# Performance work log

Hardware: AMD Instinct MI355X
Metric: run time of the kernel (lower is better)

The kernel has to match this reference:

```python
import jax, jax.numpy as jnp
import numpy as np

KERNEL = 7
PAD = 3
STRIDE = 1
DIL = 1
HEADS = 8
OUT_CH = 256


def _unfold(x, k, pad, stride, dil):
    # x: (B, C, H, W) -> (B, C*k*k, Ho, Wo); channel ordering (C, kh, kw),
    # matching torch.nn.Unfold's channel-major layout.
    return jax.lax.conv_general_dilated_patches(
        x, filter_shape=(k, k), window_strides=(stride, stride),
        padding=((pad, pad), (pad, pad)), rhs_dilation=(dil, dil))


def _conv1x1(x, w, b):
    # 1x1 conv == per-pixel matmul. w: (O, C), b: (O,)
    return jnp.einsum('bchw,oc->bohw', x, w) + b[None, :, None, None]


def setup_inputs() -> dict:
    key = jax.random.key(0)
    ks = jax.random.split(key, 11)
    B, C, H, W = 2, 256, 64, 64
    f = lambda k, sh: jax.random.normal(k, sh, dtype=jnp.float32)
    ws = 1.0 / np.sqrt(C).astype(np.float32)
    return dict(
        queries=f(ks[0], (B, C, H, W)),
        keys=f(ks[1], (B, C, H, W)),
        values=f(ks[2], (B, C, H, W)),
        wq=f(ks[3], (OUT_CH, C)) * ws, bq=f(ks[4], (OUT_CH,)) * 0.01,
        wk=f(ks[5], (OUT_CH, C)) * ws, bk=f(ks[6], (OUT_CH,)) * 0.01,
        wv=f(ks[7], (OUT_CH, C)) * ws, bv=f(ks[8], (OUT_CH,)) * 0.01,
        wo=f(ks[9], (OUT_CH, OUT_CH)) * ws, bo=f(ks[10], (OUT_CH,)) * 0.01,
    )


def reference(queries, keys, values, wq, bq, wk, bk, wv, bv, wo, bo):
    B = values.shape[0]
    d = OUT_CH // HEADS
    K2 = KERNEL * KERNEL
    q = _conv1x1(queries, wq, bq)
    k = _conv1x1(keys, wk, bk)
    v = _conv1x1(values, wv, bv)
    # query 'unfold' with kernel 1, stride STRIDE == strided subsample
    q = q[:, :, ::STRIDE, ::STRIDE]
    Ho, Wo = q.shape[-2], q.shape[-1]
    L = Ho * Wo
    q = q.reshape(B, HEADS, d, L)                                  # (B,h,d,L)
    kp = _unfold(k, KERNEL, PAD, STRIDE, DIL).reshape(B, HEADS, d, K2, L)
    vp = _unfold(v, KERNEL, PAD, STRIDE, DIL).reshape(B, HEADS, d, K2, L)
    scale = jnp.float32(1.0 / np.sqrt(OUT_CH))                     # note: sqrt(out_channels), per source
    attn = jnp.einsum('bhdl,bhdkl->bhlk', q, kp) * scale           # (B,h,L,K2)
    attn = jax.nn.softmax(attn, axis=-1)
    out = jnp.einsum('bhdkl,bhlk->bhdl', vp, attn)                 # (B,h,d,L)
    out = out.reshape(B, OUT_CH, Ho, Wo)
    return _conv1x1(out, wo, bo)
```

## Files before the change

### kernel.cpp

```cpp
#include <hip/hip_runtime.h>
#include <hip/hip_fp16.h>
#include <math.h>

#define B_ 2
#define C_ 256
#define H_ 64
#define W_ 64
#define L_ 4096
#define HEADS_ 8
#define DH_ 32
#define CG_ 8
#define K_ 7
#define PAD_ 3
#define K2_ 49
#define PW_ 70
#define PPIX_ 4900
#define PADT_ ((size_t)B_*HEADS_*CG_*PPIX_)
#define WS_STR 72

typedef _Float16 f16x8 __attribute__((ext_vector_type(8)));
typedef _Float16 h2    __attribute__((ext_vector_type(2)));
typedef float    f32x4 __attribute__((ext_vector_type(4)));

__device__ inline h2 u2h(unsigned u) { union { unsigned u; h2 h; } c; c.u = u; return c.h; }
__device__ inline h2 cvt2h(float a, float b) {
    auto r = __builtin_amdgcn_cvt_pkrtz(a, b);
    union { decltype(r) s; h2 d; } c; c.s = r; return c.d;
}
__device__ inline unsigned pkh(float a, float b) {
    union { h2 h; unsigned u; } c; c.h = cvt2h(a, b); return c.u;
}

__global__ __launch_bounds__(256) void prep(
    const float* __restrict__ wq, const float* __restrict__ wk,
    const float* __restrict__ wv, const float* __restrict__ wo,
    unsigned* __restrict__ wb)
{
    int idx = blockIdx.x*256 + threadIdx.x;
    const float* src = (idx < 32768) ? wq : (idx < 65536) ? wk : (idx < 98304) ? wv : wo;
    int off = (idx & 32767) * 2;
    wb[idx] = pkh(src[off], src[off+1]);
}

__global__ __launch_bounds__(256) void qkv_mfma(
    const float* __restrict__ q_in, const float* __restrict__ k_in, const float* __restrict__ v_in,
    const unsigned* __restrict__ wb,
    const float* __restrict__ bq, const float* __restrict__ bk, const float* __restrict__ bv,
    uint2* __restrict__ qt2, uint2* __restrict__ kt2, uint2* __restrict__ vt2)
{
    const int z = blockIdx.z;
    const int tid = threadIdx.x;

    if (z == 6) {
        const int flat = blockIdx.x + 64*blockIdx.y;
        const uint2 zz = make_uint2(0u, 0u);
        for (size_t idx = (size_t)flat*256 + tid; idx < PADT_; idx += 128*256) {
            int cell = (int)(idx % PPIX_);
            int px = cell % PW_, py = cell / PW_;
            if (px < PAD_ || px >= PW_-PAD_ || py < PAD_ || py >= PW_-PAD_) {
                kt2[idx] = zz;
                vt2[idx] = zz;
            }
        }
        return;
    }

    const int which = z >> 1;
    const int b = z & 1;
    const float* X = (which==0) ? q_in : (which==1 ? k_in : v_in);
    const unsigned* wbp = wb + which*32768;
    const float* bias = (which==0) ? bq : (which==1 ? bk : bv);

    const int y    = blockIdx.x;
    const int l0   = y * 64;
    const int o_t0 = blockIdx.y * 128;
    const int lane = tid & 63, wave = tid >> 6;
    const int orow = lane & 15, kgrp = lane >> 4;

    __shared__ _Float16 Ws[128*WS_STR];
    __shared__ _Float16 Xs[64*WS_STR];

    f32x4 acc[2][4] = {};

    for (int ch = 0; ch < 4; ++ch) {
        const int c0 = ch*64;
        #pragma unroll
        for (int i = 0; i < 8; ++i) {
            int o  = i*16 + (tid>>4);
            int c4 = tid & 15;
            uint2 v = *reinterpret_cast<const uint2*>(wbp + (size_t)(o_t0 + o)*128 + (c0>>1) + c4*2);
            *reinterpret_cast<uint2*>(&Ws[o*WS_STR + c4*4]) = v;
        }
        #pragma unroll
        for (int i = 0; i < 4; ++i) {
            int c_loc = (tid>>4) + i*16;
            int l4    = (tid&15)*4;
            float4 xv = *reinterpret_cast<const float4*>(&X[(size_t)(b*C_ + c0 + c_loc)*L_ + l0 + l4]);
            Xs[(l4+0)*WS_STR + c_loc] = (_Float16)xv.x;
            Xs[(l4+1)*WS_STR + c_loc] = (_Float16)xv.y;
            Xs[(l4+2)*WS_STR + c_loc] = (_Float16)xv.z;
            Xs[(l4+3)*WS_STR + c_loc] = (_Float16)xv.w;
        }
        __syncthreads();
        #pragma unroll
        for (int kk = 0; kk < 2; ++kk) {
            f16x8 af[2], bfr[4];
            #pragma unroll
            for (int fo = 0; fo < 2; ++fo)
                af[fo] = *reinterpret_cast<const f16x8*>(&Ws[(wave*32 + fo*16 + orow)*WS_STR + kk*32 + kgrp*8]);
            #pragma unroll
            for (int fn = 0; fn < 4; ++fn)
                bfr[fn] = *reinterpret_cast<const f16x8*>(&Xs[(fn*16 + orow)*WS_STR + kk*32 + kgrp*8]);
            #pragma unroll
            for (int fo = 0; fo < 2; ++fo)
                #pragma unroll
                for (int fn = 0; fn < 4; ++fn)
                    acc[fo][fn] = __builtin_amdgcn_mfma_f32_16x16x32_f16(af[fo], bfr[fn], acc[fo][fn], 0, 0, 0);
        }
        __syncthreads();
    }

    #pragma unroll
    for (int fo = 0; fo < 2; ++fo) {
        const int og = o_t0 + wave*32 + fo*16 + kgrp*4;
        const float4 b4 = *reinterpret_cast<const float4*>(&bias[og]);
        const size_t p = (size_t)(b*64 + (og >> 2));
        #pragma unroll
        for (int fn = 0; fn < 4; ++fn) {
            const int xl = fn*16 + orow;
            uint2 r = make_uint2(pkh(acc[fo][fn][0] + b4.x, acc[fo][fn][1] + b4.y),
                                 pkh(acc[fo][fn][2] + b4.z, acc[fo][fn][3] + b4.w));
            if (which == 0) {
                qt2[p*L_ + l0 + xl] = r;
            } else {
                uint2* dst = (which==1) ? kt2 : vt2;
                dst[p*PPIX_ + (size_t)(y+PAD_)*PW_ + (xl+PAD_)] = r;
            }
        }
    }
}

__global__ __launch_bounds__(256) void local_attn(
    uint2* __restrict__ qt2, const uint2* __restrict__ kt2, const uint2* __restrict__ vt2)
{
    const int tid = threadIdx.x;
    const int w = tid >> 6, x = tid & 63;
    const int bid = blockIdx.x;
    const int plane = bid & 15;
    const int y = bid >> 4;

    const uint2* kb = kt2 + (size_t)plane*CG_*PPIX_;
    const uint2* vb = vt2 + (size_t)plane*CG_*PPIX_;
    uint2* qpl = qt2 + (size_t)plane*CG_*L_;

    __shared__ float S[K2_][64];

    const float scale = 0.0625f;

    float lg[2][K_] = {};
    #pragma unroll
    for (int cg=0; cg<CG_; ++cg) {
        uint2 qu = qpl[(size_t)cg*L_ + y*W_ + x];
        const h2 q01 = u2h(qu.x), q23 = u2h(qu.y);
        #pragma unroll
        for (int rr=0; rr<2; ++rr) {
            const int r = w + rr*4;
            if (r > 6) continue;
            const uint2* row = kb + (size_t)cg*PPIX_ + (size_t)(y + r)*PW_ + x;
            #pragma unroll
            for (int kx=0; kx<K_; ++kx) {
                uint2 kk = row[kx];
                lg[rr][kx] = __builtin_amdgcn_fdot2(q01, u2h(kk.x), lg[rr][kx], false);
                lg[rr][kx] = __builtin_amdgcn_fdot2(q23, u2h(kk.y), lg[rr][kx], false);
            }
        }
    }
    #pragma unroll
    for (int rr=0; rr<2; ++rr) {
        const int r = w + rr*4;
        if (r <= 6) {
            #pragma unroll
            for (int kx=0; kx<K_; ++kx) S[r*K_+kx][x] = __expf(lg[rr][kx]*scale);
        }
    }
    __syncthreads();

    float sum = 0.f;
    #pragma unroll
    for (int i=0;i<K2_;++i) sum += S[i][x];
    const float inv = 1.0f/sum;

    const int cg0 = w*2, cg1 = w*2 + 1;
    float4 a0 = make_float4(0.f,0.f,0.f,0.f);
    float4 a1 = make_float4(0.f,0.f,0.f,0.f);
    #pragma unroll
    for (int r=0; r<K_; ++r) {
        const uint2* row0 = vb + (size_t)cg0*PPIX_ + (size_t)(y + r)*PW_ + x;
        const uint2* row1 = vb + (size_t)cg1*PPIX_ + (size_t)(y + r)*PW_ + x;
        h2 ra0 = (h2)0, ra1 = (h2)0, rb0 = (h2)0, rb1 = (h2)0;
        #pragma unroll
        for (int kx=0; kx<K_; ++kx) {
            const float p = S[r*K_+kx][x];
            const h2 p2 = cvt2h(p, p);
            uint2 u0 = row0[kx];
            uint2 u1 = row1[kx];
            ra0 += p2 * u2h(u0.x);
            ra1 += p2 * u2h(u0.y);
            rb0 += p2 * u2h(u1.x);
            rb1 += p2 * u2h(u1.y);
        }
        a0.x += (float)ra0[0]; a0.y += (float)ra0[1];
        a0.z += (float)ra1[0]; a0.w += (float)ra1[1];
        a1.x += (float)rb0[0]; a1.y += (float)rb0[1];
        a1.z += (float)rb1[0]; a1.w += (float)rb1[1];
    }
    qpl[(size_t)cg0*L_ + y*W_ + x] = make_uint2(pkh(a0.x*inv, a0.y*inv), pkh(a0.z*inv, a0.w*inv));
    qpl[(size_t)cg1*L_ + y*W_ + x] = make_uint2(pkh(a1.x*inv, a1.y*inv), pkh(a1.z*inv, a1.w*inv));
}

__global__ __launch_bounds__(256) void out_mfma(
    const uint2* __restrict__ qt2, const unsigned* __restrict__ wb,
    const float* __restrict__ bo, float* __restrict__ out)
{
    const int b    = blockIdx.z;
    const int l0   = blockIdx.x * 64;
    const int o_t0 = blockIdx.y * 64;
    const unsigned* wbp = wb + 3*32768;
    const int tid  = threadIdx.x;
    const int lane = tid & 63, wave = tid >> 6;
    const int orow = lane & 15, kgrp = lane >> 4;

    __shared__ _Float16 Ws[64*WS_STR];
    __shared__ _Float16 Xs[64*WS_STR];

    f32x4 acc[4] = {};
    const int cq  = tid >> 6;
    const int lst = tid & 63;

    for (int ch = 0; ch < 4; ++ch) {
        const int c0 = ch*64;
        #pragma unroll
        for (int i = 0; i < 4; ++i) {
            int o  = i*16 + (tid>>4);
            int c4 = tid & 15;
            uint2 v = *reinterpret_cast<const uint2*>(wbp + (size_t)(o_t0 + o)*128 + (c0>>1) + c4*2);
            *reinterpret_cast<uint2*>(&Ws[o*WS_STR + c4*4]) = v;
        }
        #pragma unroll
        for (int i = 0; i < 4; ++i) {
            int c4i = i*4 + cq;
            uint2 v = qt2[(size_t)(b*64 + (c0>>2) + c4i)*L_ + l0 + lst];
            *reinterpret_cast<uint2*>(&Xs[lst*WS_STR + c4i*4]) = v;
        }
        __syncthreads();
        #pragma unroll
        for (int kk = 0; kk < 2; ++kk) {
            f16x8 af, bfr[4];
            af = *reinterpret_cast<const f16x8*>(&Ws[(wave*16 + orow)*WS_STR + kk*32 + kgrp*8]);
            #pragma unroll
            for (int fn = 0; fn < 4; ++fn)
                bfr[fn] = *reinterpret_cast<const f16x8*>(&Xs[(fn*16 + orow)*WS_STR + kk*32 + kgrp*8]);
            #pragma unroll
            for (int fn = 0; fn < 4; ++fn)
                acc[fn] = __builtin_amdgcn_mfma_f32_16x16x32_f16(af, bfr[fn], acc[fn], 0, 0, 0);
        }
        __syncthreads();
    }

    {
        const int o_base = o_t0 + wave*16 + kgrp*4;
        #pragma unroll
        for (int fn = 0; fn < 4; ++fn) {
            const int xl = fn*16 + orow;
            #pragma unroll
            for (int r = 0; r < 4; ++r)
                out[(size_t)(b*C_ + o_base + r)*L_ + l0 + xl] = acc[fn][r] + bo[o_base + r];
        }
    }
}

extern "C" void kernel_launch(void* const* d_in, const int* in_sizes, int n_in,
                              void* d_out, int out_size, void* d_ws, size_t ws_size,
                              hipStream_t stream) {
    const float* queries = (const float*)d_in[0];
    const float* keys    = (const float*)d_in[1];
    const float* values  = (const float*)d_in[2];
    const float* wq = (const float*)d_in[3];
    const float* bq = (const float*)d_in[4];
    const float* wk = (const float*)d_in[5];
    const float* bk = (const float*)d_in[6];
    const float* wv = (const float*)d_in[7];
    const float* bv = (const float*)d_in[8];
    const float* wo = (const float*)d_in[9];
    const float* bo = (const float*)d_in[10];
    float* out = (float*)d_out;

    uint2* qt2 = (uint2*)d_ws;
    uint2* kt2 = qt2 + (size_t)B_*HEADS_*CG_*L_;
    uint2* vt2 = kt2 + PADT_;
    unsigned* wb = (unsigned*)(vt2 + PADT_);

    prep<<<512, 256, 0, stream>>>(wq, wk, wv, wo, wb);
    qkv_mfma<<<dim3(64, 2, 7), 256, 0, stream>>>(queries, keys, values, wb, bq, bk, bv, qt2, kt2, vt2);
    local_attn<<<1024, 256, 0, stream>>>(qt2, kt2, vt2);
    out_mfma<<<dim3(64, 4, 2), 256, 0, stream>>>(qt2, wb, bo, out);
}
```

Baseline: 52.05 us.

## Fold weight fp16 conversion into GEMM kernels and zero only padding border cells

Removes the separate prep kernel that packed all weights to fp16. The QKV and output GEMM kernels now read fp32 weights directly and convert them while staging into shared memory, which saves one launch and a workspace round trip. The border-zeroing path now walks only the 804 padding cells per plane instead of scanning every padded cell with modulo tests. In exchange, each block reads twice the weight bytes and repeats the conversion work.

```diff
diff --git a/kernel.cpp b/kernel.cpp
--- a/kernel.cpp
+++ b/kernel.cpp
@@ -31,20 +31,9 @@
     union { h2 h; unsigned u; } c; c.h = cvt2h(a, b); return c.u;
 }
 
-__global__ __launch_bounds__(256) void prep(
-    const float* __restrict__ wq, const float* __restrict__ wk,
-    const float* __restrict__ wv, const float* __restrict__ wo,
-    unsigned* __restrict__ wb)
-{
-    int idx = blockIdx.x*256 + threadIdx.x;
-    const float* src = (idx < 32768) ? wq : (idx < 65536) ? wk : (idx < 98304) ? wv : wo;
-    int off = (idx & 32767) * 2;
-    wb[idx] = pkh(src[off], src[off+1]);
-}
-
 __global__ __launch_bounds__(256) void qkv_mfma(
     const float* __restrict__ q_in, const float* __restrict__ k_in, const float* __restrict__ v_in,
-    const unsigned* __restrict__ wb,
+    const float* __restrict__ wq, const float* __restrict__ wk, const float* __restrict__ wv,
     const float* __restrict__ bq, const float* __restrict__ bk, const float* __restrict__ bv,
     uint2* __restrict__ qt2, uint2* __restrict__ kt2, uint2* __restrict__ vt2)
 {
@@ -54,22 +43,25 @@
     if (z == 6) {
         const int flat = blockIdx.x + 64*blockIdx.y;
         const uint2 zz = make_uint2(0u, 0u);
-        for (size_t idx = (size_t)flat*256 + tid; idx < PADT_; idx += 128*256) {
-            int cell = (int)(idx % PPIX_);
-            int px = cell % PW_, py = cell / PW_;
-            if (px < PAD_ || px >= PW_-PAD_ || py < PAD_ || py >= PW_-PAD_) {
-                kt2[idx] = zz;
-                vt2[idx] = zz;
-            }
+        for (int e = flat*256 + tid; e < 128*804; e += 128*256) {
+            int pl = e / 804;
+            int c  = e - pl*804;
+            int py, px;
+            if (c < 210)      { py = c/70;            px = c%70; }
+            else if (c < 420) { int c2 = c-210; py = 67 + c2/70; px = c2%70; }
+            else              { int c2 = c-420; py = 3 + c2/6; int j = c2%6; px = (j<3) ? j : 64+j; }
+            size_t idx = (size_t)pl*PPIX_ + (size_t)py*PW_ + px;
+            kt2[idx] = zz;
+            vt2[idx] = zz;
         }
         return;
     }
 
     const int which = z >> 1;
     const int b = z & 1;
-    const float* X = (which==0) ? q_in : (which==1 ? k_in : v_in);
-    const unsigned* wbp = wb + which*32768;
-    const float* bias = (which==0) ? bq : (which==1 ? bk : bv);
+    const float* X    = (which==0) ? q_in : (which==1 ? k_in : v_in);
+    const float* wsrc = (which==0) ? wq   : (which==1 ? wk   : wv);
+    const float* bias = (which==0) ? bq   : (which==1 ? bk   : bv);
 
     const int y    = blockIdx.x;
     const int l0   = y * 64;
@@ -88,8 +80,9 @@
         for (int i = 0; i < 8; ++i) {
             int o  = i*16 + (tid>>4);
             int c4 = tid & 15;
-            uint2 v = *reinterpret_cast<const uint2*>(wbp + (size_t)(o_t0 + o)*128 + (c0>>1) + c4*2);
-            *reinterpret_cast<uint2*>(&Ws[o*WS_STR + c4*4]) = v;
+            float4 wv4 = *reinterpret_cast<const float4*>(&wsrc[(size_t)(o_t0 + o)*C_ + c0 + c4*4]);
+            uint2 pk = make_uint2(pkh(wv4.x, wv4.y), pkh(wv4.z, wv4.w));
+            *reinterpret_cast<uint2*>(&Ws[o*WS_STR + c4*4]) = pk;
         }
         #pragma unroll
         for (int i = 0; i < 4; ++i) {
@@ -219,13 +212,12 @@
 }
 
 __global__ __launch_bounds__(256) void out_mfma(
-    const uint2* __restrict__ qt2, const unsigned* __restrict__ wb,
+    const uint2* __restrict__ qt2, const float* __restrict__ wo,
     const float* __restrict__ bo, float* __restrict__ out)
 {
     const int b    = blockIdx.z;
     const int l0   = blockIdx.x * 64;
     const int o_t0 = blockIdx.y * 64;
-    const unsigned* wbp = wb + 3*32768;
     const int tid  = threadIdx.x;
     const int lane = tid & 63, wave = tid >> 6;
     const int orow = lane & 15, kgrp = lane >> 4;
@@ -243,8 +235,9 @@
         for (int i = 0; i < 4; ++i) {
             int o  = i*16 + (tid>>4);
             int c4 = tid & 15;
-            uint2 v = *reinterpret_cast<const uint2*>(wbp + (size_t)(o_t0 + o)*128 + (c0>>1) + c4*2);
-            *reinterpret_cast<uint2*>(&Ws[o*WS_STR + c4*4]) = v;
+            float4 wv4 = *reinterpret_cast<const float4*>(&wo[(size_t)(o_t0 + o)*C_ + c0 + c4*4]);
+            uint2 pk = make_uint2(pkh(wv4.x, wv4.y), pkh(wv4.z, wv4.w));
+            *reinterpret_cast<uint2*>(&Ws[o*WS_STR + c4*4]) = pk;
         }
         #pragma unroll
         for (int i = 0; i < 4; ++i) {
@@ -298,10 +291,9 @@
     uint2* qt2 = (uint2*)d_ws;
     uint2* kt2 = qt2 + (size_t)B_*HEADS_*CG_*L_;
     uint2* vt2 = kt2 + PADT_;
-    unsigned* wb = (unsigned*)(vt2 + PADT_);
-
-    prep<<<512, 256, 0, stream>>>(wq, wk, wv, wo, wb);
-    qkv_mfma<<<dim3(64, 2, 7), 256, 0, stream>>>(queries, keys, values, wb, bq, bk, bv, qt2, kt2, vt2);
+
+    qkv_mfma<<<dim3(64, 2, 7), 256, 0, stream>>>(queries, keys, values,
+                                                 wq, wk, wv, bq, bk, bv, qt2, kt2, vt2);
     local_attn<<<1024, 256, 0, stream>>>(qt2, kt2, vt2);
-    out_mfma<<<dim3(64, 4, 2), 256, 0, stream>>>(qt2, wb, bo, out);
-}
+    out_mfma<<<dim3(64, 4, 2), 256, 0, stream>>>(qt2, wo, bo, out);
+}
```

Result: slower. 55.32 us (+6.3%).
